# Optimization experiments

Hardware: AMD Instinct MI355X
Metric: run time of the kernel (lower is better)

## Reference

```python
import jax, jax.numpy as jnp
import numpy as np

K = 8192  # num_embeddings
D = 256   # embedding_dim


def setup_inputs() -> dict:
    key = jax.random.key(0)
    k1, k2 = jax.random.split(key)
    z_e = jax.random.normal(k1, (16, 2048, D), dtype=jnp.float32)
    # codebook init: randn * 1/sqrt(D), matching the torch buffer init
    embedding = jax.random.normal(k2, (K, D), dtype=jnp.float32) * (1.0 / np.sqrt(D))
    return {"z_e": z_e, "embedding": embedding}


def reference(z_e, embedding):
    # Eval-mode forward of VectorQuantizerEMA (no EMA buffer update, no mask).
    B, M, Dd = z_e.shape
    Kk = embedding.shape[0]
    flat = z_e.reshape(-1, Dd)  # [N, D]

    distances = (
        jnp.sum(flat * flat, axis=1, keepdims=True)
        - 2.0 * (flat @ embedding.T)
        + jnp.sum(embedding * embedding, axis=1)[None, :]
    )
    indices = jnp.argmin(distances, axis=1)  # [N] int

    z_q = embedding[indices].reshape(B, M, Dd)
    z_q_st = z_e + jax.lax.stop_gradient(z_q - z_e)

    # instantaneous usage stats (perplexity, dead ratio)
    usage = jnp.zeros((Kk,), dtype=jnp.float32).at[indices].add(1.0)
    total = jnp.maximum(usage.sum(), 1.0)
    probs = usage / total
    safe_p = jnp.where(probs > 0, probs, 1.0)
    perplexity = jnp.exp(-jnp.sum(probs * jnp.log(safe_p)))
    dead_ratio = jnp.mean((usage == 0).astype(jnp.float32))
    stats = jnp.stack([perplexity, dead_ratio])

    return z_q_st, z_q, indices.reshape(B, M), stats
```

## Files before the change

kernel.cpp:

```cpp
#include <hip/hip_runtime.h>

#define N_ROWS 32768
#define D_DIM  256
#define K_CODES 8192

#define OUT0_OFF 0
#define OUT1_OFF 8388608
#define OUTI_OFF 16777216
#define OUTS_OFF 16809984

typedef _Float16 half4 __attribute__((ext_vector_type(4)));
typedef _Float16 half8 __attribute__((ext_vector_type(8)));
typedef float    f32x16 __attribute__((ext_vector_type(16)));

#define HN_OFF  0x400000
#define CAND_OFF 0x500000

#define MARGIN 0.05f

#define PK(v, id) __uint_as_float((__float_as_uint(v) & 0xFFFFFFC0u) | (unsigned)(id))

__global__ __launch_bounds__(256) void vq_conv(const float* __restrict__ E,
                                               const float* __restrict__ x,
                                               char* __restrict__ Estg,
                                               float* __restrict__ hn,
                                               char* __restrict__ Xh,
                                               int* __restrict__ usage) {
    if (blockIdx.x < 2048) {
        const int wv = threadIdx.x >> 6;
        const int l = threadIdx.x & 63;
        const int code = blockIdx.x * 4 + wv;
        float4 v = ((const float4*)E)[code * 64 + l];

        const int g = code >> 6, c = code & 63;
        const int st = l >> 5;
        const int dg = ((4 * l) & 127) >> 3;
        const int slot = (dg + c) & 15;
        const int sub = 8 * (l & 1);

        half4 hh = {(_Float16)v.x, (_Float16)v.y, (_Float16)v.z, (_Float16)v.w};
        char* p = Estg + (size_t)g * 32768 + st * 16384 + c * 256 + slot * 16 + sub;
        *(half4*)p = hh;

        float s = v.x * v.x + v.y * v.y + v.z * v.z + v.w * v.w;
        #pragma unroll
        for (int off = 32; off >= 1; off >>= 1) s += __shfl_down(s, off);
        if (l == 0) hn[code] = -0.5f * s;

        if (blockIdx.x < K_CODES / 256) usage[blockIdx.x * 256 + threadIdx.x] = 0;
    } else {
        const size_t i4 = ((size_t)(blockIdx.x - 2048) * 256 + threadIdx.x) * 4;
        float4 v = *(const float4*)(x + i4);
        half4 hh = {(_Float16)v.x, (_Float16)v.y, (_Float16)v.z, (_Float16)v.w};
        *(half4*)(Xh + i4 * 2) = hh;
    }
}

#define STAGE_COMPUTE(LDSOFF, KSB)                                             \
    _Pragma("unroll")                                                          \
    for (int ks = 0; ks < 8; ++ks) {                                           \
        const int slot = (2 * ks + hc) & 15;                                   \
        const int sa = rb0 + slot * 16 + (LDSOFF);                             \
        half8 a0 = *(const half8*)(lds + sa);                                  \
        half8 a1 = *(const half8*)(lds + sa + 8192);                           \
        const half8 b0 = xr0[(KSB) + ks];                                      \
        const half8 b1 = xr1[(KSB) + ks];                                      \
        acc00 = __builtin_amdgcn_mfma_f32_32x32x16_f16(a0, b0, acc00, 0, 0, 0);\
        acc01 = __builtin_amdgcn_mfma_f32_32x32x16_f16(a0, b1, acc01, 0, 0, 0);\
        acc10 = __builtin_amdgcn_mfma_f32_32x32x16_f16(a1, b0, acc10, 0, 0, 0);\
        acc11 = __builtin_amdgcn_mfma_f32_32x32x16_f16(a1, b1, acc11, 0, 0, 0);\
    }

#define ISSUE_STAGE(gsrc, BUFOFF)                                              \
    _Pragma("unroll") for (int i = 0; i < 4; ++i)                              \
        __builtin_amdgcn_global_load_lds(                                      \
            (const __attribute__((address_space(1))) void*)((gsrc) + i * 4096 + t16), \
            (__attribute__((address_space(3))) void*)(lds + (BUFOFF) + i * 4096 + t16), \
            16, 0, 0);

#define TOP2_UPD(v, cidx, T0, T1, I0, I1)                                      \
    if ((v) > (T1)) {                                                          \
        const bool g_ = (v) > (T0);                                            \
        (T1) = g_ ? (T0) : (v);                                                \
        (I1) = g_ ? (I0) : (cidx);                                             \
        if (g_) { (T0) = (v); (I0) = (cidx); }                                 \
    }

__global__ __launch_bounds__(256, 2) void vq_mfma(const char* __restrict__ Estg,
                                                  const float* __restrict__ hnp,
                                                  const char* __restrict__ Xh,
                                                  float2* __restrict__ cand) {
    __shared__ __attribute__((aligned(16))) char lds[32768];

    const int tid = threadIdx.x;
    const int w = tid >> 6, lane = tid & 63;
    const int cl = lane & 31, half = lane >> 5;
    const int t16 = tid * 16;
    const int rb0 = cl * 256;
    const int hc = half + cl;

    const int part = blockIdx.x & 3;
    const int qb = blockIdx.x >> 2;
    const char* Ebase = Estg + (size_t)part * 32 * 32768;

    const int qw = qb * 256 + w * 64;
    const char* xbA = Xh + (size_t)(qw + cl) * 512 + half * 16;
    const char* xbB = Xh + (size_t)(qw + 32 + cl) * 512 + half * 16;
    half8 xr0[16], xr1[16];
    #pragma unroll
    for (int ks = 0; ks < 16; ++ks) {
        xr0[ks] = *(const half8*)(xbA + ks * 32);
        xr1[ks] = *(const half8*)(xbB + ks * 32);
    }

    ISSUE_STAGE(Ebase, 0)

    float mA[16], mB[16];
    #pragma unroll
    for (int r = 0; r < 16; ++r) { mA[r] = -3.4e38f; mB[r] = -3.4e38f; }

    for (int g = 0; g < 32; ++g) {
        const char* egrp = Ebase + (size_t)g * 32768;
        const char* enxt = Ebase + (size_t)((g + 1) & 31) * 32768;

        f32x16 acc00 = {}, acc01 = {}, acc10 = {}, acc11 = {};

        __syncthreads();
        ISSUE_STAGE(egrp + 16384, 16384)
        const float* hq = hnp + part * 2048 + g * 64 + 4 * half;
        float4 hn0[4], hn1[4];
        #pragma unroll
        for (int j = 0; j < 4; ++j) {
            hn0[j] = *(const float4*)(hq + 8 * j);
            hn1[j] = *(const float4*)(hq + 32 + 8 * j);
        }
        STAGE_COMPUTE(0, 0)

        __syncthreads();
        ISSUE_STAGE(enxt, 0)
        STAGE_COMPUTE(16384, 8)

        const int gid2 = g * 2;
        #pragma unroll
        for (int r = 0; r < 16; ++r) {
            const float h0 = hn0[r >> 2][r & 3];
            const float h1 = hn1[r >> 2][r & 3];
            mA[r] = fmaxf(fmaxf(mA[r], PK(acc00[r] + h0, gid2)),
                          PK(acc10[r] + h1, gid2 + 1));
            mB[r] = fmaxf(fmaxf(mB[r], PK(acc01[r] + h0, gid2)),
                          PK(acc11[r] + h1, gid2 + 1));
        }
    }

    float t0a = -3.4e38f, t1a = -3.4e38f, t0b = -3.4e38f, t1b = -3.4e38f;
    int i0a = 0, i1a = 0, i0b = 0, i1b = 0;
    #pragma unroll
    for (int r = 0; r < 16; ++r) {
        const int rc = (r & 3) + 8 * (r >> 2);
        {
            const unsigned b = __float_as_uint(mA[r]);
            const int id = (int)(b & 63u);
            const int code = (id >> 1) * 64 + (id & 1) * 32 + 4 * half + rc;
            const float v = mA[r];
            TOP2_UPD(v, code, t0a, t1a, i0a, i1a);
        }
        {
            const unsigned b = __float_as_uint(mB[r]);
            const int id = (int)(b & 63u);
            const int code = (id >> 1) * 64 + (id & 1) * 32 + 4 * half + rc;
            const float v = mB[r];
            TOP2_UPD(v, code, t0b, t1b, i0b, i1b);
        }
    }

    const size_t bA = (size_t)(qw + cl) * 16 + part * 4 + half * 2;
    cand[bA]     = make_float2(t0a, __int_as_float(part * 2048 + i0a));
    cand[bA + 1] = make_float2(t1a, __int_as_float(part * 2048 + i1a));
    const size_t bB = (size_t)(qw + 32 + cl) * 16 + part * 4 + half * 2;
    cand[bB]     = make_float2(t0b, __int_as_float(part * 2048 + i0b));
    cand[bB + 1] = make_float2(t1b, __int_as_float(part * 2048 + i1b));
}

__global__ __launch_bounds__(256) void vq_resolve(const float2* __restrict__ cand,
                                                  const float* __restrict__ x,
                                                  const float* __restrict__ E,
                                                  float* __restrict__ outI,
                                                  int* __restrict__ wsIdx,
                                                  int* __restrict__ usage) {
    const int row = blockIdx.x * 4 + (threadIdx.x >> 6);
    const int lane = threadIdx.x & 63;

    float v = -3.4e38f;
    int ci = 0x7fffffff;
    if (lane < 16) {
        float2 c = cand[(size_t)row * 16 + lane];
        v = c.x;
        ci = __float_as_int(c.y);
    }
    float m = v;
    #pragma unroll
    for (int off = 8; off >= 1; off >>= 1) m = fmaxf(m, __shfl_xor(m, off, 16));
    m = __shfl(m, 0);

    const bool im = (lane < 16) && (v >= m - MARGIN);
    const unsigned long long mk = __ballot(im);
    int besti;
    if (__popcll(mk) == 1) {
        int wmin = im ? ci : 0x7fffffff;
        #pragma unroll
        for (int off = 8; off >= 1; off >>= 1)
            wmin = min(wmin, __shfl_xor(wmin, off, 16));
        besti = __shfl(wmin, 0);
    } else {
        const float4 x4 = *(const float4*)(x + (size_t)row * 256 + lane * 4);
        double bq = -1.0e300;
        besti = 0x7fffffff;
        unsigned long long mm = mk;
        while (mm) {
            const int j = __ffsll(mm) - 1;
            mm &= mm - 1;
            const int cidx = __shfl(ci, j);
            const float4 e4 = *(const float4*)(E + (size_t)cidx * 256 + lane * 4);
            double ps = (double)x4.x * e4.x + (double)x4.y * e4.y +
                        (double)x4.z * e4.z + (double)x4.w * e4.w -
                        0.5 * ((double)e4.x * e4.x + (double)e4.y * e4.y +
                               (double)e4.z * e4.z + (double)e4.w * e4.w);
            #pragma unroll
            for (int off = 32; off >= 1; off >>= 1) ps += __shfl_xor(ps, off);
            if (ps > bq || (ps == bq && cidx < besti)) { bq = ps; besti = cidx; }
        }
    }

    if (lane == 0) {
        outI[row] = (float)besti;
        wsIdx[row] = besti;
        atomicAdd(&usage[besti], 1);
    }
}

__global__ __launch_bounds__(256) void vq_gather(const int* __restrict__ wsIdx,
                                                 const float* __restrict__ E,
                                                 float* __restrict__ out0,
                                                 float* __restrict__ out1) {
    const int row = blockIdx.x * 4 + (threadIdx.x >> 6);
    const int lane = threadIdx.x & 63;
    const int idx = wsIdx[row];
    float4 e4 = ((const float4*)(E + (size_t)idx * D_DIM))[lane];
    ((float4*)(out0 + (size_t)row * D_DIM))[lane] = e4;
    ((float4*)(out1 + (size_t)row * D_DIM))[lane] = e4;
}

__global__ __launch_bounds__(1024) void vq_stats(const int* __restrict__ usage,
                                                 float* __restrict__ statsOut) {
    __shared__ float redp[1024];
    __shared__ int   redz[1024];
    const int t = threadIdx.x;
    float pl = 0.0f;
    int zc = 0;
    for (int i = t; i < K_CODES; i += 1024) {
        const int u = usage[i];
        if (u == 0) {
            zc++;
        } else {
            const float p = (float)u * (1.0f / (float)N_ROWS);
            pl += p * logf(p);
        }
    }
    redp[t] = pl;
    redz[t] = zc;
    __syncthreads();
    for (int s = 512; s > 0; s >>= 1) {
        if (t < s) { redp[t] += redp[t + s]; redz[t] += redz[t + s]; }
        __syncthreads();
    }
    if (t == 0) {
        statsOut[0] = expf(-redp[0]);
        statsOut[1] = (float)redz[0] / (float)K_CODES;
    }
}

extern "C" void kernel_launch(void* const* d_in, const int* in_sizes, int n_in,
                              void* d_out, int out_size, void* d_ws, size_t ws_size,
                              hipStream_t stream) {
    const float* z_e = (const float*)d_in[0];
    const float* E   = (const float*)d_in[1];

    float* out   = (float*)d_out;
    char*  out_b = (char*)d_out;

    char*   Estg  = out_b;
    float*  hn    = (float*)(out_b + HN_OFF);
    float2* candb = (float2*)(out_b + CAND_OFF);
    char*   Xh    = out_b + (size_t)OUT1_OFF * 4;

    float* out0 = out + OUT0_OFF;
    float* out1 = out + OUT1_OFF;
    float* outI = out + OUTI_OFF;
    float* outS = out + OUTS_OFF;

    int* usage = (int*)d_ws;
    int* wsIdx = (int*)((char*)d_ws + 32768);

    vq_conv<<<dim3(10240), dim3(256), 0, stream>>>(E, z_e, Estg, hn, Xh, usage);
    vq_mfma<<<dim3(512), dim3(256), 0, stream>>>(Estg, hn, Xh, candb);
    vq_resolve<<<dim3(8192), dim3(256), 0, stream>>>(candb, z_e, E, outI, wsIdx, usage);
    vq_gather<<<dim3(8192), dim3(256), 0, stream>>>(wsIdx, E, out0, out1);
    vq_stats<<<dim3(1), dim3(1024), 0, stream>>>(usage, outS);
}
```

Measured before the change: 272.4 us.

## Deepen codebook LDS pipeline to four stages with vmcnt-based barriers

Replaces the double-buffered codebook staging with a four-slot LDS ring holding three stages in flight. Each stage waits only on its own loads via a partial vmcnt wait before the barrier, so memory latency can hide behind more MFMA work. The per-group norm bias is preloaded into LDS once instead of read from global memory every group, and setprio raises the MFMA sections' priority. Doubling LDS to 64KB plus 8KB may cut occupancy below the two blocks per CU the launch bounds request.

```diff
diff --git a/kernel.cpp b/kernel.cpp
--- a/kernel.cpp
+++ b/kernel.cpp
@@ -71,12 +71,50 @@
         acc11 = __builtin_amdgcn_mfma_f32_32x32x16_f16(a1, b1, acc11, 0, 0, 0);\
     }
 
-#define ISSUE_STAGE(gsrc, BUFOFF)                                              \
-    _Pragma("unroll") for (int i = 0; i < 4; ++i)                              \
-        __builtin_amdgcn_global_load_lds(                                      \
-            (const __attribute__((address_space(1))) void*)((gsrc) + i * 4096 + t16), \
-            (__attribute__((address_space(3))) void*)(lds + (BUFOFF) + i * 4096 + t16), \
-            16, 0, 0);
+#define ISSUE_STAGE(SN, DSTOFF)                                                \
+    {                                                                          \
+        const char* gs_ = Ebase + (size_t)(((SN) & 63) * 16384);               \
+        _Pragma("unroll") for (int i = 0; i < 4; ++i)                          \
+            __builtin_amdgcn_global_load_lds(                                  \
+                (const __attribute__((address_space(1))) void*)(gs_ + i * 4096 + t16), \
+                (__attribute__((address_space(3))) void*)(lds + (DSTOFF) + i * 4096 + t16), \
+                16, 0, 0);                                                     \
+    }
+
+#define STAGE_SYNC_ISSUE(SN, DSTOFF)                                           \
+    asm volatile("s_waitcnt vmcnt(8)" ::: "memory");                           \
+    __builtin_amdgcn_s_barrier();                                              \
+    __builtin_amdgcn_sched_barrier(0);                                         \
+    ISSUE_STAGE(SN, DSTOFF)
+
+#define GROUP_BODY(G, SN1, DB1, SRCA, SN2, DB2, SRCB)                          \
+    {                                                                          \
+        f32x16 acc00 = {}, acc01 = {}, acc10 = {}, acc11 = {};                 \
+        STAGE_SYNC_ISSUE(SN1, DB1)                                             \
+        __builtin_amdgcn_s_setprio(1);                                         \
+        STAGE_COMPUTE(SRCA, 0)                                                 \
+        __builtin_amdgcn_s_setprio(0);                                         \
+        STAGE_SYNC_ISSUE(SN2, DB2)                                             \
+        __builtin_amdgcn_s_setprio(1);                                         \
+        STAGE_COMPUTE(SRCB, 8)                                                 \
+        __builtin_amdgcn_s_setprio(0);                                         \
+        const float4* hq4 = (const float4*)(hn_lds + (G) * 64 + 4 * half);     \
+        float4 hn0[4], hn1[4];                                                 \
+        _Pragma("unroll") for (int j = 0; j < 4; ++j) {                        \
+            hn0[j] = hq4[2 * j];                                               \
+            hn1[j] = hq4[2 * j + 8];                                           \
+        }                                                                      \
+        const int gid2 = (G) * 2;                                              \
+        _Pragma("unroll")                                                      \
+        for (int r = 0; r < 16; ++r) {                                         \
+            const float h0 = hn0[r >> 2][r & 3];                               \
+            const float h1 = hn1[r >> 2][r & 3];                               \
+            mA[r] = fmaxf(fmaxf(mA[r], PK(acc00[r] + h0, gid2)),               \
+                          PK(acc10[r] + h1, gid2 + 1));                        \
+            mB[r] = fmaxf(fmaxf(mB[r], PK(acc01[r] + h0, gid2)),               \
+                          PK(acc11[r] + h1, gid2 + 1));                        \
+        }                                                                      \
+    }
 
 #define TOP2_UPD(v, cidx, T0, T1, I0, I1)                                      \
     if ((v) > (T1)) {                                                          \
@@ -90,7 +128,8 @@
                                                   const float* __restrict__ hnp,
                                                   const char* __restrict__ Xh,
                                                   float2* __restrict__ cand) {
-    __shared__ __attribute__((aligned(16))) char lds[32768];
+    __shared__ __attribute__((aligned(16))) char lds[65536];
+    __shared__ __attribute__((aligned(16))) float hn_lds[2048];
 
     const int tid = threadIdx.x;
     const int w = tid >> 6, lane = tid & 63;
@@ -113,44 +152,28 @@
         xr1[ks] = *(const half8*)(xbB + ks * 32);
     }
 
-    ISSUE_STAGE(Ebase, 0)
+    {
+        const float4* hsrc = (const float4*)(hnp + part * 2048);
+        ((float4*)hn_lds)[tid] = hsrc[tid];
+        ((float4*)hn_lds)[tid + 256] = hsrc[tid + 256];
+    }
+    __syncthreads();
+
+    ISSUE_STAGE(0, 0)
+    ISSUE_STAGE(1, 16384)
+    ISSUE_STAGE(2, 32768)
 
     float mA[16], mB[16];
     #pragma unroll
     for (int r = 0; r < 16; ++r) { mA[r] = -3.4e38f; mB[r] = -3.4e38f; }
 
-    for (int g = 0; g < 32; ++g) {
-        const char* egrp = Ebase + (size_t)g * 32768;
-        const char* enxt = Ebase + (size_t)((g + 1) & 31) * 32768;
-
-        f32x16 acc00 = {}, acc01 = {}, acc10 = {}, acc11 = {};
-
-        __syncthreads();
-        ISSUE_STAGE(egrp + 16384, 16384)
-        const float* hq = hnp + part * 2048 + g * 64 + 4 * half;
-        float4 hn0[4], hn1[4];
-        #pragma unroll
-        for (int j = 0; j < 4; ++j) {
-            hn0[j] = *(const float4*)(hq + 8 * j);
-            hn1[j] = *(const float4*)(hq + 32 + 8 * j);
-        }
-        STAGE_COMPUTE(0, 0)
-
-        __syncthreads();
-        ISSUE_STAGE(enxt, 0)
-        STAGE_COMPUTE(16384, 8)
-
-        const int gid2 = g * 2;
-        #pragma unroll
-        for (int r = 0; r < 16; ++r) {
-            const float h0 = hn0[r >> 2][r & 3];
-            const float h1 = hn1[r >> 2][r & 3];
-            mA[r] = fmaxf(fmaxf(mA[r], PK(acc00[r] + h0, gid2)),
-                          PK(acc10[r] + h1, gid2 + 1));
-            mB[r] = fmaxf(fmaxf(mB[r], PK(acc01[r] + h0, gid2)),
-                          PK(acc11[r] + h1, gid2 + 1));
-        }
-    }
+    #pragma unroll 1
+    for (int gg = 0; gg < 16; ++gg) {
+        const int s0 = 4 * gg;
+        GROUP_BODY(2 * gg,     s0 + 3, 49152, 0,     s0 + 4, 0,     16384)
+        GROUP_BODY(2 * gg + 1, s0 + 5, 16384, 32768, s0 + 6, 32768, 49152)
+    }
+    asm volatile("s_waitcnt vmcnt(0)" ::: "memory");
 
     float t0a = -3.4e38f, t1a = -3.4e38f, t0b = -3.4e38f, t1b = -3.4e38f;
     int i0a = 0, i1a = 0, i0b = 0, i1b = 0;
```

New measurement: 496.7 us. +82.3%, slower.
